# Optimization experiments

Measured on AMD Instinct MI355X. Metric: run time of the kernel, lower is better.

## Reference

```python
import jax, jax.numpy as jnp
import numpy as np

NUM_NODES = 128
TEMPERATURE = 1.0
NEG = -1e30  # stand-in for -inf that is safe under softmax/grad


def setup_inputs() -> dict:
    key = jax.random.key(0)
    k1, k2, k3 = jax.random.split(key, 3)
    D, N = 1024, NUM_NODES
    P = jax.random.normal(k1, (N, N), jnp.float32)
    P = P.at[jnp.arange(N), jnp.arange(N)].set(-50.0)  # fill_diagonal_(-50)
    uniforms = jax.random.uniform(k2, (D, N), jnp.float32)       # categorical sampling draws
    gumbel_u = jax.random.uniform(k3, (D, 2, N, N), jnp.float32)  # gumbel-softmax base uniforms
    return {"P": P, "uniforms": uniforms, "gumbel_u": gumbel_u, "num_dags": D}


def reference(P, uniforms, gumbel_u, num_dags):
    N = P.shape[0]
    D = uniforms.shape[0]
    sigP = jax.nn.sigmoid(P)  # [N,N], shared across all dags

    # --- Phase 1: sequential node-ordering sampling (mask-based, fixed shapes) ---
    def step(active, u):
        # active: [D,N] bool, True = node still remaining
        masked = jnp.where(active[:, None, :], sigP[None, :, :], NEG)  # [D,N,N]
        row_max = masked.max(-1)                                       # max over remaining cols
        logits = jnp.where(active, (1.0 - row_max) / TEMPERATURE, NEG)
        probs = jax.nn.softmax(logits, axis=-1)                        # softmax over remaining rows
        cum = jnp.cumsum(probs, -1)
        cond = (cum >= u[:, None]) & active
        idx = jnp.argmax(cond, -1)
        last_active = (N - 1) - jnp.argmax(active[:, ::-1], -1)
        idx = jnp.where(cond.any(-1), idx, last_active)  # fp fallback
        active = active & (jnp.arange(N)[None, :] != idx[:, None])
        return active, idx

    active0 = jnp.ones((D, N), dtype=bool)
    _, order_T = jax.lax.scan(step, active0, uniforms.T)  # scan over N steps
    order = order_T.T  # [D,N]

    # --- Phase 2: permute, lower-triangular, gumbel-softmax, unpermute ---
    Ap = sigP[order[:, :, None], order[:, None, :]]  # [D,N,N] = sigP[order_i, order_j]
    tril_mask = jnp.tril(jnp.ones((N, N), dtype=bool), -1)
    A_low = jnp.where(tril_mask, Ap, 0.0)
    logA = jnp.where(tril_mask, jnp.log(jnp.where(tril_mask, Ap, 1.0)), NEG)
    log1mA = jnp.log1p(-A_low)
    logits2 = jnp.stack([logA, log1mA], axis=1)  # [D,2,N,N]
    g = -jnp.log(-jnp.log(gumbel_u + 1e-10) + 1e-10)
    y_soft = jax.nn.softmax(logits2 + g, axis=1)  # tau = 1 (torch default)
    am = jnp.argmax(y_soft, axis=1)  # [D,N,N]
    hard = (am[:, None, :, :] == jnp.arange(2)[None, :, None, None]).astype(y_soft.dtype)
    y = jax.lax.stop_gradient(hard - y_soft) + y_soft  # straight-through
    Y = y[:, 0]  # [D,N,N]

    # undo permutation: out[d, order[i], order[j]] = Y[d, i, j]
    inv = jnp.argsort(order, axis=-1)
    unperm = jax.vmap(lambda m, p: m[p][:, p])(Y, inv)
    return unperm.transpose(0, 2, 1), order
```

## Files before the change

### kernel.cpp

```cpp
#include <hip/hip_runtime.h>

#define NN 128
#define NEGF -1e30f
#define DELTA 1.5e-5f

__device__ __forceinline__ float dpp_scan_add(float x) {
    int v;
    v = __builtin_amdgcn_update_dpp(0, __float_as_int(x), 0x111, 0xf, 0xf, true);
    x += __int_as_float(v);
    v = __builtin_amdgcn_update_dpp(0, __float_as_int(x), 0x112, 0xf, 0xf, true);
    x += __int_as_float(v);
    v = __builtin_amdgcn_update_dpp(0, __float_as_int(x), 0x114, 0xf, 0xf, true);
    x += __int_as_float(v);
    v = __builtin_amdgcn_update_dpp(0, __float_as_int(x), 0x118, 0xf, 0xf, true);
    x += __int_as_float(v);
    v = __builtin_amdgcn_update_dpp(0, __float_as_int(x), 0x142, 0xa, 0xf, true);
    x += __int_as_float(v);
    v = __builtin_amdgcn_update_dpp(0, __float_as_int(x), 0x143, 0xc, 0xf, true);
    x += __int_as_float(v);
    return x;
}

__device__ __forceinline__ float dpp_scan_max(float x) {
    const int negi = __float_as_int(NEGF);
    int v;
    v = __builtin_amdgcn_update_dpp(negi, __float_as_int(x), 0x111, 0xf, 0xf, false);
    x = fmaxf(x, __int_as_float(v));
    v = __builtin_amdgcn_update_dpp(negi, __float_as_int(x), 0x112, 0xf, 0xf, false);
    x = fmaxf(x, __int_as_float(v));
    v = __builtin_amdgcn_update_dpp(negi, __float_as_int(x), 0x114, 0xf, 0xf, false);
    x = fmaxf(x, __int_as_float(v));
    v = __builtin_amdgcn_update_dpp(negi, __float_as_int(x), 0x118, 0xf, 0xf, false);
    x = fmaxf(x, __int_as_float(v));
    v = __builtin_amdgcn_update_dpp(negi, __float_as_int(x), 0x142, 0xa, 0xf, false);
    x = fmaxf(x, __int_as_float(v));
    v = __builtin_amdgcn_update_dpp(negi, __float_as_int(x), 0x143, 0xc, 0xf, false);
    x = fmaxf(x, __int_as_float(v));
    return x;
}

__device__ __forceinline__ float bcast63(float x) {
    return __int_as_float(__builtin_amdgcn_readlane(__float_as_int(x), 63));
}

__global__ void k_sig(const float* __restrict__ P, float* __restrict__ sigS) {
    int i = blockIdx.x * blockDim.x + threadIdx.x;
    if (i < NN * NN) {
        double p = (double)P[i];
        sigS[i] = (float)(1.0 / (1.0 + exp(-p)));
    }
}

__launch_bounds__(256)
__global__ void k_fused(const float* __restrict__ sigS,
                        const float* __restrict__ uniforms,
                        const float* __restrict__ G,
                        float* __restrict__ out0,
                        float* __restrict__ orderF, int D) {
    __shared__ float S[NN * NN];
    __shared__ unsigned char T8[4][NN * NN];
    __shared__ int ordS[4 * NN];
    const int tid = threadIdx.x;

    for (int k = 0; k < 16; ++k) {
        int idx4 = (k * 256 + tid) * 4;
        int r = idx4 >> 7, cb = idx4 & 127;
        float4 v = *reinterpret_cast<const float4*>(&sigS[idx4]);
        int x = r & 31;
        float4 w;
        switch (x & 3) {
            case 0: w = v; break;
            case 1: w = make_float4(v.y, v.x, v.w, v.z); break;
            case 2: w = make_float4(v.z, v.w, v.x, v.y); break;
            default: w = make_float4(v.w, v.z, v.y, v.x); break;
        }
        *reinterpret_cast<float4*>(&S[r * 128 + ((cb ^ x) & ~3)]) = w;
    }
    {
        uint4 z = make_uint4(0, 0, 0, 0);
        #pragma unroll
        for (int k = 0; k < 16; ++k)
            reinterpret_cast<uint4*>(&T8[0][0])[k * 256 + tid] = z;
    }
    __syncthreads();

    const int lane = tid & 63;
    const int wv = tid >> 6;
    const int dag = blockIdx.x * 4 + wv;

    if (dag < D) {
        const int i0 = 2 * lane, i1 = 2 * lane + 1;
        const int x0 = i0 & 31, x1 = i1 & 31;
        const int q0 = x0 & 3, q1 = x1 & 3;
        float2 uu = *reinterpret_cast<const float2*>(&uniforms[dag * NN + i0]);

        unsigned long long mlo = ~0ull, mhi = ~0ull;

        float rm0 = NEGF, rm1 = NEGF;
        int rc0 = 0, rc1 = 0;
        for (int k = 0; k < 32; ++k) {
            int cb = 4 * ((k + lane) & 31);
            float4 a = *reinterpret_cast<const float4*>(&S[i0 * 128 + (cb ^ (x0 & ~3))]);
            float4 b = *reinterpret_cast<const float4*>(&S[i1 * 128 + (cb ^ (x1 & ~3))]);
            if (a.x > rm0) { rm0 = a.x; rc0 = cb | (0 ^ q0); }
            if (a.y > rm0) { rm0 = a.y; rc0 = cb | (1 ^ q0); }
            if (a.z > rm0) { rm0 = a.z; rc0 = cb | (2 ^ q0); }
            if (a.w > rm0) { rm0 = a.w; rc0 = cb | (3 ^ q0); }
            if (b.x > rm1) { rm1 = b.x; rc1 = cb | (0 ^ q1); }
            if (b.y > rm1) { rm1 = b.y; rc1 = cb | (1 ^ q1); }
            if (b.z > rm1) { rm1 = b.z; rc1 = cb | (2 ^ q1); }
            if (b.w > rm1) { rm1 = b.w; rc1 = cb | (3 ^ q1); }
        }

        float e0 = __expf(1.0f - rm0);
        float e1 = __expf(1.0f - rm1);

        #pragma unroll 1
        for (int t = 0; t < NN; ++t) {
            float usel = (t & 1) ? uu.y : uu.x;
            float ut = __int_as_float(__builtin_amdgcn_readlane(__float_as_int(usel), t >> 1));

            float incl = dpp_scan_add(e0 + e1);
            float T = bcast63(incl);
            float thr = ut * T;
            float cum1 = incl, cum0 = incl - e1;

            bool a0 = (e0 != 0.0f), a1 = (e1 != 0.0f);
            bool c0 = a0 && (cum0 >= thr);
            bool c1 = a1 && (cum1 >= thr);
            float mg = DELTA * T;
            bool amb = (a0 && fabsf(cum0 - thr) <= mg) || (a1 && fabsf(cum1 - thr) <= mg);

            unsigned long long b0 = __ballot(c0), b1 = __ballot(c1);
            unsigned long long ba = __ballot(amb);
            int lastActive = mhi ? (127 - __clzll(mhi)) : (63 - __clzll(mlo));

            int idx;
            if (__builtin_expect(ba != 0ull, 0)) {
                float l0 = 1.0f - rm0, l1v = 1.0f - rm1;
                float lvi = fmaxf(a0 ? l0 : NEGF, a1 ? l1v : NEGF);
                float lv = bcast63(dpp_scan_max(lvi));
                float f0 = a0 ? expf(l0 - lv) : 0.0f;
                float f1 = a1 ? expf(l1v - lv) : 0.0f;
                int mm = lane & 3;
                float s0 = __shfl(f0, mm), s1 = __shfl(f1, mm);
                #pragma unroll
                for (int k2 = 1; k2 < 16; ++k2) {
                    s0 += __shfl(f0, mm + 4 * k2);
                    s1 += __shfl(f1, mm + 4 * k2);
                }
                float A00 = __shfl(s0, 0), A01 = __shfl(s0, 1), A02 = __shfl(s0, 2), A03 = __shfl(s0, 3);
                float A10 = __shfl(s1, 0), A11 = __shfl(s1, 1), A12 = __shfl(s1, 2), A13 = __shfl(s1, 3);
                float tot = ((A00 + A10) + (A01 + A11)) + ((A02 + A12) + (A03 + A13));
                float s = 0.0f;
                int pick = -1;
                for (int j = 0; j < NN; ++j) {
                    float ej = __shfl((j & 1) ? f1 : f0, j >> 1);
                    float pj = ej / tot;
                    s += pj;
                    bool aj = (j < 64) ? ((mlo >> j) & 1ull) : ((mhi >> (j - 64)) & 1ull);
                    if (pick < 0 && aj && s >= ut) pick = j;
                }
                idx = (pick >= 0) ? pick : lastActive;
            } else {
                int f0i = b0 ? 2 * (__ffsll(b0) - 1) : 999;
                int f1i = b1 ? 2 * (__ffsll(b1) - 1) + 1 : 999;
                idx = min(f0i, f1i);
                if (idx == 999) idx = lastActive;
            }

            if (lane == 0) ordS[wv * NN + t] = idx;

            if (idx < 64) mlo &= ~(1ull << idx);
            else          mhi &= ~(1ull << (idx - 64));
            if (idx == i0) e0 = 0.0f;
            if (idx == i1) e1 = 0.0f;
            a0 = (e0 != 0.0f); a1 = (e1 != 0.0f);

            unsigned long long r0 = __ballot(a0 && (rc0 == idx));
            unsigned long long r1 = __ballot(a1 && (rc1 == idx));

            while (r0) {
                int L = __ffsll(r0) - 1; r0 &= r0 - 1;
                int row = 2 * L, xm = row & 31;
                float v0 = ((mlo >> lane) & 1) ? S[row * 128 + (lane ^ xm)] : NEGF;
                float v1 = ((mhi >> lane) & 1) ? S[row * 128 + ((lane + 64) ^ xm)] : NEGF;
                float m2 = bcast63(dpp_scan_max(fmaxf(v0, v1)));
                unsigned long long h0 = __ballot(v0 == m2);
                unsigned long long h1 = __ballot(v1 == m2);
                int nc = h0 ? (__ffsll(h0) - 1) : (64 + __ffsll(h1) - 1);
                if (lane == L) { rm0 = m2; rc0 = nc; e0 = __expf(1.0f - m2); }
            }
            while (r1) {
                int L = __ffsll(r1) - 1; r1 &= r1 - 1;
                int row = 2 * L + 1, xm = row & 31;
                float v0 = ((mlo >> lane) & 1) ? S[row * 128 + (lane ^ xm)] : NEGF;
                float v1 = ((mhi >> lane) & 1) ? S[row * 128 + ((lane + 64) ^ xm)] : NEGF;
                float m2 = bcast63(dpp_scan_max(fmaxf(v0, v1)));
                unsigned long long h0 = __ballot(v0 == m2);
                unsigned long long h1 = __ballot(v1 == m2);
                int nc = h0 ? (__ffsll(h0) - 1) : (64 + __ffsll(h1) - 1);
                if (lane == L) { rm1 = m2; rc1 = nc; e1 = __expf(1.0f - m2); }
            }
        }
    }
    __syncthreads();

    #pragma unroll
    for (int k = 0; k < 2; ++k) {
        int i = k * 256 + tid;
        int dg = blockIdx.x * 4 + (i >> 7);
        if (dg < D) orderF[(size_t)blockIdx.x * 512 + i] = (float)ordS[i];
    }

    for (int w = 0; w <= 4; ++w) {
        if (w >= 1) {
            const int dPrev = blockIdx.x * 4 + (w - 1);
            if (dPrev < D) {
                const unsigned char* Tp = T8[w - 1];
                float* od = out0 + (size_t)dPrev * NN * NN;
                #pragma unroll
                for (int k = 0; k < 16; ++k) {
                    int base = k * 1024 + tid * 4;
                    int i = base >> 7, j = base & 127;
                    const uchar4 v = *reinterpret_cast<const uchar4*>(&Tp[i * NN + (j ^ (i & 124))]);
                    float4 o;
                    o.x = (float)v.x; o.y = (float)v.y; o.z = (float)v.z; o.w = (float)v.w;
                    *reinterpret_cast<float4*>(&od[base]) = o;
                }
            }
        }
        if (w < 4) {
            const int d = blockIdx.x * 4 + w;
            if (d < D) {
                unsigned char* Tw = T8[w];
                const float* G0 = G + (size_t)d * 2 * NN * NN;
                const float* G1 = G0 + NN * NN;
                const int* pw = &ordS[w * NN];

                for (int base = 0; base < 8192; base += 2048) {
                    float u0[8], u1[8], sg[8];
                    int rr8[8], cc8[8];
                    bool ok[8];
                    #pragma unroll
                    for (int j = 0; j < 8; ++j) {
                        int k = base + j * 256 + tid;
                        ok[j] = (k < 8128);
                        if (ok[j]) {
                            float fr = sqrtf(8.0f * (float)k + 1.0f);
                            int r = (int)((1.0f + fr) * 0.5f);
                            if (r * (r - 1) / 2 > k) --r;
                            if ((r + 1) * r / 2 <= k) ++r;
                            int c = k - r * (r - 1) / 2;
                            rr8[j] = r; cc8[j] = c;
                            int idx = r * NN + c;
                            u0[j] = G0[idx];
                            u1[j] = G1[idx];
                            int prr = pw[r], pcc = pw[c];
                            sg[j] = S[prr * 128 + (pcc ^ (prr & 31))];
                        }
                    }
                    #pragma unroll
                    for (int j = 0; j < 8; ++j) {
                        if (ok[j]) {
                            int prr = pw[rr8[j]], pcc = pw[cc8[j]];
                            float A = -__logf(u0[j] + 1e-10f) + 1e-10f;
                            float B = -__logf(u1[j] + 1e-10f) + 1e-10f;
                            Tw[pcc * NN + (prr ^ (pcc & 124))] = (sg[j] * B >= (1.0f - sg[j]) * A) ? 1 : 0;
                        }
                    }
                }
            }
        }
        __syncthreads();
    }
}

extern "C" void kernel_launch(void* const* d_in, const int* in_sizes, int n_in,
                              void* d_out, int out_size, void* d_ws, size_t ws_size,
                              hipStream_t stream) {
    const float* P        = (const float*)d_in[0];
    const float* uniforms = (const float*)d_in[1];
    const float* G        = (const float*)d_in[2];
    const int D = in_sizes[1] / NN;

    float* out0   = (float*)d_out;
    float* orderF = out0 + (size_t)D * NN * NN;
    float* sigS   = (float*)d_ws;

    k_sig<<<(NN * NN + 255) / 256, 256, 0, stream>>>(P, sigS);
    k_fused<<<(D + 3) / 4, 256, 0, stream>>>(sigS, uniforms, G, out0, orderF, D);
}
```

Before: 146.7 us.

## Replace per-step row-max rescans with presorted per-row column queues

A new pre-kernel ranks each row of sigmoid(P) and writes a sorted (value, column) table in rank-major order. The fused kernel loads this table into shared memory and keeps a small register queue per row, refilled in chunks of 8. When a row's current argmax column is removed, the queue advances to the next still-active column instead of doing a wave-wide max reduction over the whole row. In exchange the table takes 128KB of shared memory, which is reused afterwards for the T8 buffers. The phase-2 gather of sigS now reads from global memory instead of shared memory, which may add latency.

```diff
diff --git a/kernel.cpp b/kernel.cpp
--- a/kernel.cpp
+++ b/kernel.cpp
@@ -3,6 +3,7 @@
 #define NN 128
 #define NEGF -1e30f
 #define DELTA 1.5e-5f
+#define Q 8
 
 __device__ __forceinline__ float dpp_scan_add(float x) {
     int v;
@@ -43,44 +44,40 @@
     return __int_as_float(__builtin_amdgcn_readlane(__float_as_int(x), 63));
 }
 
-__global__ void k_sig(const float* __restrict__ P, float* __restrict__ sigS) {
-    int i = blockIdx.x * blockDim.x + threadIdx.x;
-    if (i < NN * NN) {
-        double p = (double)P[i];
-        sigS[i] = (float)(1.0 / (1.0 + exp(-p)));
-    }
+__launch_bounds__(NN)
+__global__ void k_sort(const float* __restrict__ P, float* __restrict__ sigS,
+                       unsigned long long* __restrict__ PRg) {
+    __shared__ float row[NN];
+    const int r = blockIdx.x, c = threadIdx.x;
+    double pv = (double)P[r * NN + c];
+    float s = (float)(1.0 / (1.0 + exp(-pv)));
+    sigS[r * NN + c] = s;
+    row[c] = s;
+    __syncthreads();
+    int rank = 0;
+    for (int j = 0; j < NN; ++j) {
+        float v = row[j];
+        rank += (v > s) || (v == s && j < c);
+    }
+    PRg[rank * NN + r] = ((unsigned long long)(unsigned)__float_as_int(s) << 32) | (unsigned)c;
 }
 
 __launch_bounds__(256)
-__global__ void k_fused(const float* __restrict__ sigS,
+__global__ void k_fused(const unsigned long long* __restrict__ PRg,
+                        const float* __restrict__ sigS,
                         const float* __restrict__ uniforms,
                         const float* __restrict__ G,
                         float* __restrict__ out0,
                         float* __restrict__ orderF, int D) {
-    __shared__ float S[NN * NN];
-    __shared__ unsigned char T8[4][NN * NN];
+    __shared__ unsigned long long PR[NN * NN];
     __shared__ int ordS[4 * NN];
     const int tid = threadIdx.x;
 
-    for (int k = 0; k < 16; ++k) {
-        int idx4 = (k * 256 + tid) * 4;
-        int r = idx4 >> 7, cb = idx4 & 127;
-        float4 v = *reinterpret_cast<const float4*>(&sigS[idx4]);
-        int x = r & 31;
-        float4 w;
-        switch (x & 3) {
-            case 0: w = v; break;
-            case 1: w = make_float4(v.y, v.x, v.w, v.z); break;
-            case 2: w = make_float4(v.z, v.w, v.x, v.y); break;
-            default: w = make_float4(v.w, v.z, v.y, v.x); break;
-        }
-        *reinterpret_cast<float4*>(&S[r * 128 + ((cb ^ x) & ~3)]) = w;
-    }
     {
-        uint4 z = make_uint4(0, 0, 0, 0);
+        const uint4* s4 = (const uint4*)PRg;
+        uint4* d4 = (uint4*)PR;
         #pragma unroll
-        for (int k = 0; k < 16; ++k)
-            reinterpret_cast<uint4*>(&T8[0][0])[k * 256 + tid] = z;
+        for (int k = 0; k < 32; ++k) d4[k * 256 + tid] = s4[k * 256 + tid];
     }
     __syncthreads();
 
@@ -90,28 +87,23 @@
 
     if (dag < D) {
         const int i0 = 2 * lane, i1 = 2 * lane + 1;
-        const int x0 = i0 & 31, x1 = i1 & 31;
-        const int q0 = x0 & 3, q1 = x1 & 3;
         float2 uu = *reinterpret_cast<const float2*>(&uniforms[dag * NN + i0]);
 
         unsigned long long mlo = ~0ull, mhi = ~0ull;
 
-        float rm0 = NEGF, rm1 = NEGF;
-        int rc0 = 0, rc1 = 0;
-        for (int k = 0; k < 32; ++k) {
-            int cb = 4 * ((k + lane) & 31);
-            float4 a = *reinterpret_cast<const float4*>(&S[i0 * 128 + (cb ^ (x0 & ~3))]);
-            float4 b = *reinterpret_cast<const float4*>(&S[i1 * 128 + (cb ^ (x1 & ~3))]);
-            if (a.x > rm0) { rm0 = a.x; rc0 = cb | (0 ^ q0); }
-            if (a.y > rm0) { rm0 = a.y; rc0 = cb | (1 ^ q0); }
-            if (a.z > rm0) { rm0 = a.z; rc0 = cb | (2 ^ q0); }
-            if (a.w > rm0) { rm0 = a.w; rc0 = cb | (3 ^ q0); }
-            if (b.x > rm1) { rm1 = b.x; rc1 = cb | (0 ^ q1); }
-            if (b.y > rm1) { rm1 = b.y; rc1 = cb | (1 ^ q1); }
-            if (b.z > rm1) { rm1 = b.z; rc1 = cb | (2 ^ q1); }
-            if (b.w > rm1) { rm1 = b.w; rc1 = cb | (3 ^ q1); }
+        float qv0[Q], qv1[Q];
+        int qc0[Q], qc1[Q];
+        #pragma unroll
+        for (int j = 0; j < Q; ++j) {
+            unsigned long long e0j = PR[j * NN + i0];
+            unsigned long long e1j = PR[j * NN + i1];
+            qv0[j] = __int_as_float((int)(e0j >> 32)); qc0[j] = (int)(e0j & 127u);
+            qv1[j] = __int_as_float((int)(e1j >> 32)); qc1[j] = (int)(e1j & 127u);
         }
-
+        int pos0 = Q, pos1 = Q;
+        int rem0 = Q, rem1 = Q;
+
+        float rm0 = qv0[0], rm1 = qv1[0];
         float e0 = __expf(1.0f - rm0);
         float e1 = __expf(1.0f - rm1);
 
@@ -175,32 +167,46 @@
             else          mhi &= ~(1ull << (idx - 64));
             if (idx == i0) e0 = 0.0f;
             if (idx == i1) e1 = 0.0f;
-            a0 = (e0 != 0.0f); a1 = (e1 != 0.0f);
-
-            unsigned long long r0 = __ballot(a0 && (rc0 == idx));
-            unsigned long long r1 = __ballot(a1 && (rc1 == idx));
-
-            while (r0) {
-                int L = __ffsll(r0) - 1; r0 &= r0 - 1;
-                int row = 2 * L, xm = row & 31;
-                float v0 = ((mlo >> lane) & 1) ? S[row * 128 + (lane ^ xm)] : NEGF;
-                float v1 = ((mhi >> lane) & 1) ? S[row * 128 + ((lane + 64) ^ xm)] : NEGF;
-                float m2 = bcast63(dpp_scan_max(fmaxf(v0, v1)));
-                unsigned long long h0 = __ballot(v0 == m2);
-                unsigned long long h1 = __ballot(v1 == m2);
-                int nc = h0 ? (__ffsll(h0) - 1) : (64 + __ffsll(h1) - 1);
-                if (lane == L) { rm0 = m2; rc0 = nc; e0 = __expf(1.0f - m2); }
-            }
-            while (r1) {
-                int L = __ffsll(r1) - 1; r1 &= r1 - 1;
-                int row = 2 * L + 1, xm = row & 31;
-                float v0 = ((mlo >> lane) & 1) ? S[row * 128 + (lane ^ xm)] : NEGF;
-                float v1 = ((mhi >> lane) & 1) ? S[row * 128 + ((lane + 64) ^ xm)] : NEGF;
-                float m2 = bcast63(dpp_scan_max(fmaxf(v0, v1)));
-                unsigned long long h0 = __ballot(v0 == m2);
-                unsigned long long h1 = __ballot(v1 == m2);
-                int nc = h0 ? (__ffsll(h0) - 1) : (64 + __ffsll(h1) - 1);
-                if (lane == L) { rm1 = m2; rc1 = nc; e1 = __expf(1.0f - m2); }
+
+            if (e0 != 0.0f && qc0[0] == idx) {
+                for (;;) {
+                    #pragma unroll
+                    for (int j = 0; j < Q - 1; ++j) { qv0[j] = qv0[j + 1]; qc0[j] = qc0[j + 1]; }
+                    if (--rem0 == 0) {
+                        #pragma unroll
+                        for (int j = 0; j < Q; ++j) {
+                            int k = min(pos0 + j, NN - 1);
+                            unsigned long long e = PR[k * NN + i0];
+                            qv0[j] = __int_as_float((int)(e >> 32));
+                            qc0[j] = (int)(e & 127u);
+                        }
+                        pos0 += Q; rem0 = Q;
+                    }
+                    int hc = qc0[0];
+                    bool act = (hc < 64) ? ((mlo >> hc) & 1ull) : ((mhi >> (hc - 64)) & 1ull);
+                    if (act) break;
+                }
+                rm0 = qv0[0]; e0 = __expf(1.0f - rm0);
+            }
+            if (e1 != 0.0f && qc1[0] == idx) {
+                for (;;) {
+                    #pragma unroll
+                    for (int j = 0; j < Q - 1; ++j) { qv1[j] = qv1[j + 1]; qc1[j] = qc1[j + 1]; }
+                    if (--rem1 == 0) {
+                        #pragma unroll
+                        for (int j = 0; j < Q; ++j) {
+                            int k = min(pos1 + j, NN - 1);
+                            unsigned long long e = PR[k * NN + i1];
+                            qv1[j] = __int_as_float((int)(e >> 32));
+                            qc1[j] = (int)(e & 127u);
+                        }
+                        pos1 += Q; rem1 = Q;
+                    }
+                    int hc = qc1[0];
+                    bool act = (hc < 64) ? ((mlo >> hc) & 1ull) : ((mhi >> (hc - 64)) & 1ull);
+                    if (act) break;
+                }
+                rm1 = qv1[0]; e1 = __expf(1.0f - rm1);
             }
         }
     }
@@ -213,11 +219,20 @@
         if (dg < D) orderF[(size_t)blockIdx.x * 512 + i] = (float)ordS[i];
     }
 
+    unsigned char* T8base = (unsigned char*)PR;
+    {
+        uint4 z = make_uint4(0, 0, 0, 0);
+        #pragma unroll
+        for (int k = 0; k < 16; ++k)
+            reinterpret_cast<uint4*>(T8base)[k * 256 + tid] = z;
+    }
+    __syncthreads();
+
     for (int w = 0; w <= 4; ++w) {
         if (w >= 1) {
             const int dPrev = blockIdx.x * 4 + (w - 1);
             if (dPrev < D) {
-                const unsigned char* Tp = T8[w - 1];
+                const unsigned char* Tp = T8base + (w - 1) * NN * NN;
                 float* od = out0 + (size_t)dPrev * NN * NN;
                 #pragma unroll
                 for (int k = 0; k < 16; ++k) {
@@ -233,7 +248,7 @@
         if (w < 4) {
             const int d = blockIdx.x * 4 + w;
             if (d < D) {
-                unsigned char* Tw = T8[w];
+                unsigned char* Tw = T8base + w * NN * NN;
                 const float* G0 = G + (size_t)d * 2 * NN * NN;
                 const float* G1 = G0 + NN * NN;
                 const int* pw = &ordS[w * NN];
@@ -256,8 +271,7 @@
                             int idx = r * NN + c;
                             u0[j] = G0[idx];
                             u1[j] = G1[idx];
-                            int prr = pw[r], pcc = pw[c];
-                            sg[j] = S[prr * 128 + (pcc ^ (prr & 31))];
+                            sg[j] = sigS[pw[r] * NN + pw[c]];
                         }
                     }
                     #pragma unroll
@@ -287,7 +301,8 @@
     float* out0   = (float*)d_out;
     float* orderF = out0 + (size_t)D * NN * NN;
     float* sigS   = (float*)d_ws;
-
-    k_sig<<<(NN * NN + 255) / 256, 256, 0, stream>>>(P, sigS);
-    k_fused<<<(D + 3) / 4, 256, 0, stream>>>(sigS, uniforms, G, out0, orderF, D);
-}
+    unsigned long long* PRg = (unsigned long long*)((char*)d_ws + 65536);
+
+    k_sort<<<NN, NN, 0, stream>>>(P, sigS, PRg);
+    k_fused<<<(D + 3) / 4, 256, 0, stream>>>(PRg, sigS, uniforms, G, out0, orderF, D);
+}
```

Measured after the change: 176.6 us. +20.4%, slower.
